# Optimization experiments

Hardware: AMD Instinct MI355X
Metric: run time of the kernel (lower is better)

## Reference

```python
import jax, jax.numpy as jnp
import numpy as np

NUM_TAG = 128
T, B = 1024, 512


def setup_inputs() -> dict:
    key = jax.random.key(0)
    k_em, k_tag, k_s, k_t, k_e = jax.random.split(key, 5)
    emissions = jax.random.normal(k_em, (T, B, NUM_TAG), dtype=jnp.float32)
    tags = jax.random.randint(k_tag, (T, B), 0, NUM_TAG, dtype=jnp.int32)
    mask = jnp.ones((T, B), dtype=jnp.float32)
    # parameters: uniform(-0.1, 0.1) as in reset_params
    start_transitions = jax.random.uniform(k_s, (NUM_TAG,), minval=-0.1, maxval=0.1, dtype=jnp.float32)
    transitions = jax.random.uniform(k_t, (NUM_TAG, NUM_TAG), minval=-0.1, maxval=0.1, dtype=jnp.float32)
    end_transitions = jax.random.uniform(k_e, (NUM_TAG,), minval=-0.1, maxval=0.1, dtype=jnp.float32)
    return {
        "emissions": emissions,
        "tags": tags,
        "mask": mask,
        "start_transitions": start_transitions,
        "transitions": transitions,
        "end_transitions": end_transitions,
    }


def _path_score(emissions, tags, mask, start_transitions, transitions, end_transitions):
    # emissions: [T,B,K], tags/mask: [T,B]
    b_idx = jnp.arange(tags.shape[1])
    # emission score of the gold tag at each step: [T,B]
    em_tag = jnp.take_along_axis(emissions, tags[:, :, None].astype(jnp.int32), axis=2)[:, :, 0]
    scores = start_transitions[tags[0]] + (em_tag * mask).sum(axis=0)
    # transition scores along the gold path, masked: [T-1,B]
    scores = scores + (transitions[tags[:-1], tags[1:]] * mask[1:]).sum(axis=0)
    last_idx = mask.astype(jnp.int32).sum(axis=0) - 1  # [B]
    last_tag = tags[last_idx, b_idx]
    return scores + end_transitions[last_tag]


def _log_partition(emissions, mask, start_transitions, transitions, end_transitions):
    log_prob0 = start_transitions[None, :] + emissions[0]  # [B,K]

    def step(log_prob, xs):
        em_t, m_t = xs  # [B,K], [B]
        # score[b,i,j] = log_prob[b,i] + transitions[i,j] + em_t[b,j]
        score = jax.nn.logsumexp(
            log_prob[:, :, None] + transitions[None, :, :] + em_t[:, None, :], axis=1
        )
        new_lp = score * m_t[:, None] + log_prob * (1.0 - m_t)[:, None]
        return new_lp, None

    log_prob, _ = jax.lax.scan(step, log_prob0, (emissions[1:], mask[1:]))
    return jax.nn.logsumexp(log_prob + end_transitions[None, :], axis=1)  # [B]


def reference(emissions, tags, mask, start_transitions, transitions, end_transitions):
    path = _path_score(emissions, tags, mask, start_transitions, transitions, end_transitions)
    log_z = _log_partition(emissions, mask, start_transitions, transitions, end_transitions)
    return (path - log_z).sum()
```

## Files before the change

### kernel.cpp

```cpp
#include <hip/hip_runtime.h>
#include <cstdint>

#define TT 1024
#define BB 512
#define KK 128
#define XPAD 132
#define NSLOT 8

typedef __attribute__((ext_vector_type(8))) short short8;
typedef __attribute__((ext_vector_type(4))) float f4;
typedef __attribute__((ext_vector_type(4))) unsigned int uint4v;

__device__ __forceinline__ unsigned short f2bf_rtne(float x) {
  unsigned u = __float_as_uint(x);
  u += 0x7FFF + ((u >> 16) & 1);
  return (unsigned short)(u >> 16);
}

__device__ __forceinline__ unsigned pack_trunc(float l, float h) {
  return __builtin_amdgcn_perm(__float_as_uint(h), __float_as_uint(l), 0x07060302u);
}

__device__ __forceinline__ void lgkm_barrier() {
  __atomic_signal_fence(__ATOMIC_SEQ_CST);
  __builtin_amdgcn_s_waitcnt(0xC07F);
  __builtin_amdgcn_s_barrier();
  __atomic_signal_fence(__ATOMIC_SEQ_CST);
}

__global__ __launch_bounds__(128, 1) void crf_forward(
    const float* __restrict__ em, const float* __restrict__ mask,
    const float* __restrict__ start_t, const float* __restrict__ trans,
    const float* __restrict__ end_t, float* __restrict__ logz)
{
  const int tid  = threadIdx.x;
  const int wid  = tid >> 6;
  const int lane = tid & 63;
  const int q    = lane >> 4;
  const int lo   = lane & 15;
  const int b0   = blockIdx.x * 16;

  __shared__ __align__(16) float Xs[NSLOT][16][XPAD];

  const size_t TS = (size_t)BB * KK;
  const float* emlane = em + (size_t)(b0 + lo) * KK + 4 * q;
  const float* mrow   = mask + (b0 + lo);

  short8 Af[8][4];
  f4 S[8];
  uint4v PB[4];
  float base = 0.f, mvPrev = 1.0f;

  f4 LA[8], LB[8], LC[8], LD[8];
  float mA = 0.f, mB = 0.f, mC = 0.f, mD = 0.f;

  if (wid == 0) {
#pragma unroll
    for (int mt = 0; mt < 8; ++mt)
#pragma unroll
      for (int kt = 0; kt < 4; ++kt) {
        short8 v;
#pragma unroll
        for (int j = 0; j < 8; ++j) {
          const int ck = 32 * kt + 16 * (j >> 2) + 4 * q + (j & 3);
          v[j] = (short)f2bf_rtne(__expf(trans[(size_t)ck * KK + 16 * mt + lo]));
        }
        Af[mt][kt] = v;
      }
#pragma unroll
    for (int mt = 0; mt < 8; ++mt) {
      const f4 e0 = *(const f4*)(emlane + 16 * mt);
      const f4 st = *(const f4*)(start_t + 16 * mt + 4 * q);
#pragma unroll
      for (int i = 0; i < 4; ++i) S[mt][i] = __expf(st[i] + e0[i]);
    }
#pragma unroll
    for (int kt = 0; kt < 4; ++kt) {
      PB[kt][0] = pack_trunc(S[2 * kt][0],     S[2 * kt][1]);
      PB[kt][1] = pack_trunc(S[2 * kt][2],     S[2 * kt][3]);
      PB[kt][2] = pack_trunc(S[2 * kt + 1][0], S[2 * kt + 1][1]);
      PB[kt][3] = pack_trunc(S[2 * kt + 1][2], S[2 * kt + 1][3]);
    }
  } else {
#pragma unroll
    for (int mt = 0; mt < 8; ++mt) {
      LA[mt] = *(const f4*)(emlane + 1 * TS + 16 * mt);
      LB[mt] = *(const f4*)(emlane + 2 * TS + 16 * mt);
      LC[mt] = *(const f4*)(emlane + 3 * TS + 16 * mt);
      LD[mt] = *(const f4*)(emlane + 4 * TS + 16 * mt);
    }
    mA = mrow[1 * BB]; mB = mrow[2 * BB]; mC = mrow[3 * BB]; mD = mrow[4 * BB];
  }

  auto PROD = [&](const int t, f4 (&Ls)[8], float& ms) {
    if (t > TT) return;
    float* xb = &Xs[t & 7][lo][0];
#pragma unroll
    for (int mt = 0; mt < 8; ++mt) {
      f4 x;
#pragma unroll
      for (int i = 0; i < 4; ++i) x[i] = __expf(Ls[mt][i]);
      *(f4*)(xb + 16 * mt + 4 * q) = x;
    }
    if (q == 0) xb[128] = (t <= TT - 1) ? ms : 0.f;
    const int tp = (t + 4 <= TT - 1) ? (t + 4) : (TT - 1);
#pragma unroll
    for (int mt = 0; mt < 8; ++mt)
      Ls[mt] = *(const f4*)(emlane + (size_t)tp * TS + 16 * mt);
    ms = mrow[(size_t)tp * BB];
  };

  auto CONS = [&](const int t, const bool scale_cand, const bool do_renorm) {
    const float* xb = &Xs[t & 7][lo][0];
    f4 X[8];
#pragma unroll
    for (int mt = 0; mt < 8; ++mt) X[mt] = *(const f4*)(xb + 16 * mt + 4 * q);
    const float mk = xb[128];

    float ps = 1.0f, kln2 = 0.f;
    if (scale_cand) {
      const int k = (int)(__float_as_uint(mvPrev) >> 23) - 127;
      ps = __uint_as_float((unsigned)(127 - k) << 23);
      kln2 = (float)k * 0.6931471805599453f;
    }

    short8 Bf[4];
#pragma unroll
    for (int kt = 0; kt < 4; ++kt) Bf[kt] = __builtin_bit_cast(short8, PB[kt]);

    f4 acc[8];
#pragma unroll
    for (int mt = 0; mt < 8; ++mt) acc[mt] = f4{0.f, 0.f, 0.f, 0.f};
#pragma unroll
    for (int kt = 0; kt < 4; ++kt)
#pragma unroll
      for (int mt = 0; mt < 8; ++mt)
        acc[mt] = __builtin_amdgcn_mfma_f32_16x16x32_bf16(Af[mt][kt], Bf[kt], acc[mt], 0, 0, 0);

    const bool upd = (mk != 0.f);
#pragma unroll
    for (int mt = 0; mt < 8; ++mt)
#pragma unroll
      for (int i = 0; i < 4; ++i) {
        float n = acc[mt][i] * X[mt][i];
        if (scale_cand) n *= ps;
        S[mt][i] = upd ? n : S[mt][i];
      }
    if (scale_cand && upd) base += kln2;

#pragma unroll
    for (int kt = 0; kt < 4; ++kt) {
      PB[kt][0] = pack_trunc(S[2 * kt][0],     S[2 * kt][1]);
      PB[kt][1] = pack_trunc(S[2 * kt][2],     S[2 * kt][3]);
      PB[kt][2] = pack_trunc(S[2 * kt + 1][0], S[2 * kt + 1][1]);
      PB[kt][3] = pack_trunc(S[2 * kt + 1][2], S[2 * kt + 1][3]);
    }

    if (do_renorm) {
      float mv = S[0][0];
#pragma unroll
      for (int mt = 0; mt < 8; ++mt)
#pragma unroll
        for (int i = 0; i < 4; ++i) mv = fmaxf(mv, S[mt][i]);
      mv = fmaxf(mv, __shfl_xor(mv, 16));
      mv = fmaxf(mv, __shfl_xor(mv, 32));
      mvPrev = mv;
    }
  };

  if (wid == 1) { PROD(1, LA, mA); PROD(2, LB, mB); PROD(3, LC, mC); PROD(4, LD, mD); }
  lgkm_barrier();

  if (wid == 0) {
    CONS(1, false, false); CONS(2, false, false);
    CONS(3, false, false); CONS(4, false, true);
  } else {
    PROD(5, LA, mA); PROD(6, LB, mB); PROD(7, LC, mC); PROD(8, LD, mD);
  }
  lgkm_barrier();

  for (int g = 1; g < 256; ++g) {
    const int t0 = 4 * g;
    if (wid == 0) {
      CONS(t0 + 1, true,  false);
      CONS(t0 + 2, false, false);
      CONS(t0 + 3, false, false);
      CONS(t0 + 4, false, true);
    } else {
      PROD(t0 + 5, LA, mA); PROD(t0 + 6, LB, mB);
      PROD(t0 + 7, LC, mC); PROD(t0 + 8, LD, mD);
    }
    lgkm_barrier();
  }

  if (wid == 0) {
    float s = 0.f;
#pragma unroll
    for (int mt = 0; mt < 8; ++mt) {
      const f4 ed = *(const f4*)(end_t + 16 * mt + 4 * q);
#pragma unroll
      for (int i = 0; i < 4; ++i) s += S[mt][i] * __expf(ed[i]);
    }
    s += __shfl_xor(s, 16);
    s += __shfl_xor(s, 32);
    if (q == 0) logz[b0 + lo] = base + logf(s);
  }
}

__global__ __launch_bounds__(512) void crf_path_tb(
    const float* __restrict__ em, const int* __restrict__ tags,
    const float* __restrict__ mask, const float* __restrict__ trans,
    float* __restrict__ ws_tb)
{
  const int t = blockIdx.x, b = threadIdx.x;
  const int tg = tags[t * BB + b];
  const float mk = mask[t * BB + b];
  float v = em[((size_t)t * BB + b) * KK + tg] * mk;
  if (t >= 1) {
    const int tgp = tags[(t - 1) * BB + b];
    v += trans[(size_t)tgp * KK + tg] * mk;
  }
  __shared__ float red[8];
#pragma unroll
  for (int off = 32; off; off >>= 1) v += __shfl_xor(v, off);
  if ((b & 63) == 0) red[b >> 6] = v;
  __syncthreads();
  if (b == 0) {
    float s = 0.f;
#pragma unroll
    for (int i = 0; i < 8; ++i) s += red[i];
    ws_tb[t] = s;
  }
}

__global__ __launch_bounds__(64) void crf_bterm(
    const int* __restrict__ tags, const float* __restrict__ mask,
    const float* __restrict__ start_t, const float* __restrict__ end_t,
    float* __restrict__ ws_bt)
{
  const int b = blockIdx.x, tid = threadIdx.x;
  float ms = 0.f;
  for (int t = tid; t < TT; t += 64) ms += mask[t * BB + b];
#pragma unroll
  for (int off = 32; off; off >>= 1) ms += __shfl_xor(ms, off);
  if (tid == 0) {
    const int last = (int)(ms + 0.5f) - 1;
    ws_bt[b] = start_t[tags[b]] + end_t[tags[(size_t)last * BB + b]];
  }
}

__global__ __launch_bounds__(1024) void crf_final(
    const float* __restrict__ ws_tb, const float* __restrict__ ws_bt,
    const float* __restrict__ ws_lz, float* __restrict__ out)
{
  const int tid = threadIdx.x;
  float v = ws_tb[tid];
  if (tid < BB) v += ws_bt[tid] - ws_lz[tid];
  __shared__ float red[16];
#pragma unroll
  for (int off = 32; off; off >>= 1) v += __shfl_xor(v, off);
  if ((tid & 63) == 0) red[tid >> 6] = v;
  __syncthreads();
  if (tid == 0) {
    float s = 0.f;
#pragma unroll
    for (int i = 0; i < 16; ++i) s += red[i];
    out[0] = s;
  }
}

extern "C" void kernel_launch(void* const* d_in, const int* in_sizes, int n_in,
                              void* d_out, int out_size, void* d_ws, size_t ws_size,
                              hipStream_t stream) {
  (void)in_sizes; (void)n_in; (void)out_size; (void)ws_size;
  const float* em    = (const float*)d_in[0];
  const int*   tags  = (const int*)  d_in[1];
  const float* mask  = (const float*)d_in[2];
  const float* st    = (const float*)d_in[3];
  const float* trans = (const float*)d_in[4];
  const float* et    = (const float*)d_in[5];
  float* out = (float*)d_out;

  float* ws_tb = (float*)d_ws;
  float* ws_bt = ws_tb + 1024;
  float* ws_lz = ws_bt + 512;

  crf_path_tb<<<TT, 512, 0, stream>>>(em, tags, mask, trans, ws_tb);
  crf_bterm  <<<BB, 64, 0, stream>>>(tags, mask, st, et, ws_bt);
  crf_forward<<<32, 128, 0, stream>>>(em, mask, st, trans, et, ws_lz);
  crf_final  <<<1, 1024, 0, stream>>>(ws_tb, ws_bt, ws_lz, out);
}
```

Baseline: 1.164 ms.

## Fuse gold-path scoring into forward kernel via third wavefront

```diff
diff --git a/kernel.cpp b/kernel.cpp
--- a/kernel.cpp
+++ b/kernel.cpp
@@ -28,10 +28,11 @@
   __atomic_signal_fence(__ATOMIC_SEQ_CST);
 }
 
-__global__ __launch_bounds__(128, 1) void crf_forward(
+__global__ __launch_bounds__(192, 1) void crf_forward(
     const float* __restrict__ em, const float* __restrict__ mask,
     const float* __restrict__ start_t, const float* __restrict__ trans,
-    const float* __restrict__ end_t, float* __restrict__ logz)
+    const float* __restrict__ end_t, const int* __restrict__ tags,
+    float* __restrict__ logz, float* __restrict__ ws_path)
 {
   const int tid  = threadIdx.x;
   const int wid  = tid >> 6;
@@ -54,6 +55,9 @@
   f4 LA[8], LB[8], LC[8], LD[8];
   float mA = 0.f, mB = 0.f, mC = 0.f, mD = 0.f;
 
+  float pacc = 0.f, msum = 0.f, mkP = 0.f;
+  int tgC = 0, tpC = 0;
+
   if (wid == 0) {
 #pragma unroll
     for (int mt = 0; mt < 8; ++mt)
@@ -81,7 +85,7 @@
       PB[kt][2] = pack_trunc(S[2 * kt + 1][0], S[2 * kt + 1][1]);
       PB[kt][3] = pack_trunc(S[2 * kt + 1][2], S[2 * kt + 1][3]);
     }
-  } else {
+  } else if (wid == 1) {
 #pragma unroll
     for (int mt = 0; mt < 8; ++mt) {
       LA[mt] = *(const f4*)(emlane + 1 * TS + 16 * mt);
@@ -90,6 +94,11 @@
       LD[mt] = *(const f4*)(emlane + 4 * TS + 16 * mt);
     }
     mA = mrow[1 * BB]; mB = mrow[2 * BB]; mC = mrow[3 * BB]; mD = mrow[4 * BB];
+  } else {
+    const int rowg = b0 + lo;
+    tgC = tags[q * BB + rowg];
+    tpC = (q >= 1) ? tags[(q - 1) * BB + rowg] : 0;
+    mkP = mask[q * BB + rowg];
   }
 
   auto PROD = [&](const int t, f4 (&Ls)[8], float& ms) {
@@ -110,43 +119,31 @@
     ms = mrow[(size_t)tp * BB];
   };
 
-  auto CONS = [&](const int t, const bool scale_cand, const bool do_renorm) {
-    const float* xb = &Xs[t & 7][lo][0];
-    f4 X[8];
-#pragma unroll
-    for (int mt = 0; mt < 8; ++mt) X[mt] = *(const f4*)(xb + 16 * mt + 4 * q);
-    const float mk = xb[128];
-
-    float ps = 1.0f, kln2 = 0.f;
-    if (scale_cand) {
-      const int k = (int)(__float_as_uint(mvPrev) >> 23) - 127;
-      ps = __uint_as_float((unsigned)(127 - k) << 23);
-      kln2 = (float)k * 0.6931471805599453f;
-    }
-
+  auto CONS = [&](const f4 (&X)[8], const float mk, const bool scb,
+                  const float kln2, const bool rn) {
     short8 Bf[4];
 #pragma unroll
     for (int kt = 0; kt < 4; ++kt) Bf[kt] = __builtin_bit_cast(short8, PB[kt]);
 
     f4 acc[8];
 #pragma unroll
-    for (int mt = 0; mt < 8; ++mt) acc[mt] = f4{0.f, 0.f, 0.f, 0.f};
-#pragma unroll
-    for (int kt = 0; kt < 4; ++kt)
+    for (int mt = 0; mt < 8; ++mt)
+      acc[mt] = __builtin_amdgcn_mfma_f32_16x16x32_bf16(
+          Af[mt][0], Bf[0], f4{0.f, 0.f, 0.f, 0.f}, 0, 0, 0);
+#pragma unroll
+    for (int kt = 1; kt < 4; ++kt)
 #pragma unroll
       for (int mt = 0; mt < 8; ++mt)
         acc[mt] = __builtin_amdgcn_mfma_f32_16x16x32_bf16(Af[mt][kt], Bf[kt], acc[mt], 0, 0, 0);
 
     const bool upd = (mk != 0.f);
 #pragma unroll
-    for (int mt = 0; mt < 8; ++mt)
-#pragma unroll
-      for (int i = 0; i < 4; ++i) {
-        float n = acc[mt][i] * X[mt][i];
-        if (scale_cand) n *= ps;
-        S[mt][i] = upd ? n : S[mt][i];
-      }
-    if (scale_cand && upd) base += kln2;
+    for (int mt = 0; mt < 8; ++mt) {
+      const f4 n = acc[mt] * X[mt];
+#pragma unroll
+      for (int i = 0; i < 4; ++i) S[mt][i] = upd ? n[i] : S[mt][i];
+    }
+    if (scb && upd) base += kln2;
 
 #pragma unroll
     for (int kt = 0; kt < 4; ++kt) {
@@ -156,12 +153,11 @@
       PB[kt][3] = pack_trunc(S[2 * kt + 1][2], S[2 * kt + 1][3]);
     }
 
-    if (do_renorm) {
-      float mv = S[0][0];
-#pragma unroll
-      for (int mt = 0; mt < 8; ++mt)
-#pragma unroll
-        for (int i = 0; i < 4; ++i) mv = fmaxf(mv, S[mt][i]);
+    if (rn) {
+      float mv = fmaxf(fmaxf(S[0][0], S[0][1]), fmaxf(S[0][2], S[0][3]));
+#pragma unroll
+      for (int mt = 1; mt < 8; ++mt)
+        mv = fmaxf(mv, fmaxf(fmaxf(S[mt][0], S[mt][1]), fmaxf(S[mt][2], S[mt][3])));
       mv = fmaxf(mv, __shfl_xor(mv, 16));
       mv = fmaxf(mv, __shfl_xor(mv, 32));
       mvPrev = mv;
@@ -171,24 +167,57 @@
   if (wid == 1) { PROD(1, LA, mA); PROD(2, LB, mB); PROD(3, LC, mC); PROD(4, LD, mD); }
   lgkm_barrier();
 
-  if (wid == 0) {
-    CONS(1, false, false); CONS(2, false, false);
-    CONS(3, false, false); CONS(4, false, true);
-  } else {
-    PROD(5, LA, mA); PROD(6, LB, mB); PROD(7, LC, mC); PROD(8, LD, mD);
-  }
-  lgkm_barrier();
-
-  for (int g = 1; g < 256; ++g) {
-    const int t0 = 4 * g;
+  for (int g = 0; g < 256; ++g) {
     if (wid == 0) {
-      CONS(t0 + 1, true,  false);
-      CONS(t0 + 2, false, false);
-      CONS(t0 + 3, false, false);
-      CONS(t0 + 4, false, true);
-    } else {
+      const int t0 = 4 * g;
+      float ps = 1.f, kln2 = 0.f;
+      const bool sc = (g >= 1);
+      if (sc) {
+        const int k = (int)(__float_as_uint(mvPrev) >> 23) - 127;
+        ps = __uint_as_float((unsigned)(127 - k) << 23);
+        kln2 = (float)k * 0.6931471805599453f;
+      }
+      f4 XA[8], XB[8], XC[8], XD[8];
+      const float* x1 = &Xs[(t0 + 1) & 7][lo][0];
+      const float* x2 = &Xs[(t0 + 2) & 7][lo][0];
+      const float* x3 = &Xs[(t0 + 3) & 7][lo][0];
+      const float* x4 = &Xs[(t0 + 4) & 7][lo][0];
+#pragma unroll
+      for (int mt = 0; mt < 8; ++mt) {
+        XA[mt] = *(const f4*)(x1 + 16 * mt + 4 * q);
+        XB[mt] = *(const f4*)(x2 + 16 * mt + 4 * q);
+        XC[mt] = *(const f4*)(x3 + 16 * mt + 4 * q);
+        XD[mt] = *(const f4*)(x4 + 16 * mt + 4 * q);
+      }
+      const float mk1 = x1[128], mk2 = x2[128], mk3 = x3[128], mk4 = x4[128];
+      if (sc) {
+#pragma unroll
+        for (int mt = 0; mt < 8; ++mt) XA[mt] *= ps;
+      }
+      CONS(XA, mk1, sc, kln2, false);
+      CONS(XB, mk2, false, 0.f, false);
+      CONS(XC, mk3, false, 0.f, false);
+      CONS(XD, mk4, false, 0.f, true);
+    } else if (wid == 1) {
+      const int t0 = 4 * g;
       PROD(t0 + 5, LA, mA); PROD(t0 + 6, LB, mB);
       PROD(t0 + 7, LC, mC); PROD(t0 + 8, LD, mD);
+    } else {
+      const int t    = 4 * g + q;
+      const int rowg = b0 + lo;
+      int tgN = 0, tpN = 0; float mkN = 0.f;
+      if (g + 1 < 256) {
+        const int tn = t + 4;
+        tgN = tags[tn * BB + rowg];
+        tpN = tags[(tn - 1) * BB + rowg];
+        mkN = mask[tn * BB + rowg];
+      }
+      const float ev   = em[((size_t)t * BB + rowg) * KK + tgC];
+      const float tv   = trans[(size_t)tpC * KK + tgC];
+      const float tsel = (t > 0) ? mkP : 0.f;
+      pacc += ev * mkP + tv * tsel;
+      msum += mkP;
+      tgC = tgN; tpC = tpN; mkP = mkN;
     }
     lgkm_barrier();
   }
@@ -204,59 +233,25 @@
     s += __shfl_xor(s, 16);
     s += __shfl_xor(s, 32);
     if (q == 0) logz[b0 + lo] = base + logf(s);
-  }
-}
-
-__global__ __launch_bounds__(512) void crf_path_tb(
-    const float* __restrict__ em, const int* __restrict__ tags,
-    const float* __restrict__ mask, const float* __restrict__ trans,
-    float* __restrict__ ws_tb)
-{
-  const int t = blockIdx.x, b = threadIdx.x;
-  const int tg = tags[t * BB + b];
-  const float mk = mask[t * BB + b];
-  float v = em[((size_t)t * BB + b) * KK + tg] * mk;
-  if (t >= 1) {
-    const int tgp = tags[(t - 1) * BB + b];
-    v += trans[(size_t)tgp * KK + tg] * mk;
-  }
-  __shared__ float red[8];
-#pragma unroll
-  for (int off = 32; off; off >>= 1) v += __shfl_xor(v, off);
-  if ((b & 63) == 0) red[b >> 6] = v;
-  __syncthreads();
-  if (b == 0) {
-    float s = 0.f;
-#pragma unroll
-    for (int i = 0; i < 8; ++i) s += red[i];
-    ws_tb[t] = s;
-  }
-}
-
-__global__ __launch_bounds__(64) void crf_bterm(
-    const int* __restrict__ tags, const float* __restrict__ mask,
-    const float* __restrict__ start_t, const float* __restrict__ end_t,
-    float* __restrict__ ws_bt)
-{
-  const int b = blockIdx.x, tid = threadIdx.x;
-  float ms = 0.f;
-  for (int t = tid; t < TT; t += 64) ms += mask[t * BB + b];
-#pragma unroll
-  for (int off = 32; off; off >>= 1) ms += __shfl_xor(ms, off);
-  if (tid == 0) {
-    const int last = (int)(ms + 0.5f) - 1;
-    ws_bt[b] = start_t[tags[b]] + end_t[tags[(size_t)last * BB + b]];
-  }
-}
-
-__global__ __launch_bounds__(1024) void crf_final(
-    const float* __restrict__ ws_tb, const float* __restrict__ ws_bt,
-    const float* __restrict__ ws_lz, float* __restrict__ out)
+  } else if (wid == 2) {
+    float pa = pacc + __shfl_xor(pacc, 16); pa += __shfl_xor(pa, 32);
+    float mz = msum + __shfl_xor(msum, 16); mz += __shfl_xor(mz, 32);
+    if (q == 0) {
+      const int rowg = b0 + lo;
+      const int last = (int)(mz + 0.5f) - 1;
+      ws_path[rowg] = pa + start_t[tags[rowg]] +
+                      end_t[tags[(size_t)last * BB + rowg]];
+    }
+  }
+}
+
+__global__ __launch_bounds__(512) void crf_final(
+    const float* __restrict__ ws_path, const float* __restrict__ ws_lz,
+    float* __restrict__ out)
 {
   const int tid = threadIdx.x;
-  float v = ws_tb[tid];
-  if (tid < BB) v += ws_bt[tid] - ws_lz[tid];
-  __shared__ float red[16];
+  float v = ws_path[tid] - ws_lz[tid];
+  __shared__ float red[8];
 #pragma unroll
   for (int off = 32; off; off >>= 1) v += __shfl_xor(v, off);
   if ((tid & 63) == 0) red[tid >> 6] = v;
@@ -264,7 +259,7 @@
   if (tid == 0) {
     float s = 0.f;
 #pragma unroll
-    for (int i = 0; i < 16; ++i) s += red[i];
+    for (int i = 0; i < 8; ++i) s += red[i];
     out[0] = s;
   }
 }
@@ -281,12 +276,9 @@
   const float* et    = (const float*)d_in[5];
   float* out = (float*)d_out;
 
-  float* ws_tb = (float*)d_ws;
-  float* ws_bt = ws_tb + 1024;
-  float* ws_lz = ws_bt + 512;
-
-  crf_path_tb<<<TT, 512, 0, stream>>>(em, tags, mask, trans, ws_tb);
-  crf_bterm  <<<BB, 64, 0, stream>>>(tags, mask, st, et, ws_bt);
-  crf_forward<<<32, 128, 0, stream>>>(em, mask, st, trans, et, ws_lz);
-  crf_final  <<<1, 1024, 0, stream>>>(ws_tb, ws_bt, ws_lz, out);
-}
+  float* ws_path = (float*)d_ws;
+  float* ws_lz   = ws_path + 512;
+
+  crf_forward<<<32, 192, 0, stream>>>(em, mask, st, trans, et, tags, ws_lz, ws_path);
+  crf_final  <<<1, 512, 0, stream>>>(ws_path, ws_lz, out);
+}
```

New measurement: 2.047 ms. +75.9%, slower.
